# Performance work log

Hardware: AMD Instinct MI355X
Metric: run time of the kernel (lower is better)

Reference implementation:

```python
import jax, jax.numpy as jnp
import numpy as np

N = 100000
E = 1600000
C_IN = 32
C_OUT = 64
B = 4
VOXEL_SIZE = 0.0625
GRID_LO, GRID_HI = 0.0, 1.0
VOX = int((GRID_HI - GRID_LO) / VOXEL_SIZE)  # 16
R_CORR = GRID_HI - GRID_LO  # r_correction = max(grid_scale) - min(grid_scale) = 1


def setup_inputs() -> dict:
    key = jax.random.key(0)
    k1, k2, k3, k4, k5, k6 = jax.random.split(key, 6)
    x = jax.random.normal(k1, (N, C_IN), dtype=jnp.float32)
    edge_index = jax.random.randint(k2, (2, E), 0, N, dtype=jnp.int32)
    pos = jax.random.uniform(k3, (N, 2), dtype=jnp.float32)
    batch = jnp.sort(jax.random.randint(k4, (N,), 0, B, dtype=jnp.int32))
    W = jax.random.normal(k5, (C_OUT, 4 * C_IN), dtype=jnp.float32) / np.sqrt(4 * C_IN)
    b = jax.random.normal(k6, (C_OUT,), dtype=jnp.float32) * 0.01
    return {"x": x, "edge_index": edge_index, "pos": pos, "batch": batch, "W": W, "b": b}


def dpo_conv(x, edge_index, pos, W, b):
    row, col = edge_index[0], edge_index[1]  # j = source, i = target (PyG default flow)
    pos_i, pos_j = pos[col], pos[row]        # [E, 2]
    v_i, v_j = x[col], x[row]                # [E, C_IN]
    diff = pos_i - pos_j                     # [E, 2]
    r2 = jnp.sum(diff * diff, axis=1, keepdims=True)  # [E, 1]
    w = diff * R_CORR / (r2 + 0.01)          # [E, 2] -> columns are diff_x, diff_y
    v_diff = v_i - v_j                       # [E, C_IN]
    # message f: [E, 3*C_IN]
    f = jnp.concatenate([v_diff * w[:, 0:1], v_diff * w[:, 1:2], v_j], axis=1)
    # scatter-mean into target nodes i = col
    summed = jax.ops.segment_sum(f, col, num_segments=N)            # [N, 3*C_IN]
    cnt = jax.ops.segment_sum(jnp.ones((E, 1), f.dtype), col, num_segments=N)
    prop = summed / jnp.maximum(cnt, 1.0)
    prop = jnp.concatenate([prop, x], axis=1)  # [N, 4*C_IN]
    return prop @ W.T + b


def reference(x, edge_index, pos, batch, W, b):
    h = jax.nn.relu(dpo_conv(x, edge_index, pos, W, b))  # [N, C_OUT]
    # voxel_grid: per-graph voxel cluster ids, then max_pool per cluster (dense grid)
    vox = jnp.clip(jnp.floor((pos - GRID_LO) / VOXEL_SIZE).astype(jnp.int32), 0, VOX - 1)
    cluster = batch * (VOX * VOX) + vox[:, 1] * VOX + vox[:, 0]     # [N]
    n_clusters = B * VOX * VOX
    pooled_x = jax.ops.segment_max(h, cluster, num_segments=n_clusters)  # [B*V^2, C_OUT]
    pooled_x = jnp.where(jnp.isfinite(pooled_x), pooled_x, 0.0)          # empty voxels -> 0
    pos_sum = jax.ops.segment_sum(pos, cluster, num_segments=n_clusters)
    node_cnt = jax.ops.segment_sum(jnp.ones((N, 1), pos.dtype), cluster, num_segments=n_clusters)
    pooled_pos = pos_sum / jnp.maximum(node_cnt, 1.0)                    # mean pos per voxel
    return pooled_x, pooled_pos, pos, batch
```

## Files before the change

kernel.cpp:

```cpp
#include <hip/hip_runtime.h>

#define NN 100000
#define NE 1600000
#define CAP 64
#define NCLUST 1024
#define OUT_POOLED_POS 65536
#define OUT_POS        67584
#define OUT_BATCH      267584

__global__ __launch_bounds__(256) void fill_kernel(const int* __restrict__ ei,
                                                   int* __restrict__ wp,
                                                   int* __restrict__ csr)
{
    int t = blockIdx.x * 256 + threadIdx.x;
    int e0 = t * 4;
    if (e0 + 3 < NE) {
        int4 r = *(const int4*)(ei + e0);
        int4 c = *(const int4*)(ei + NE + e0);
        int s;
        s = atomicAdd(&wp[c.x], 1); if (s < CAP) csr[(size_t)c.x * CAP + s] = r.x;
        s = atomicAdd(&wp[c.y], 1); if (s < CAP) csr[(size_t)c.y * CAP + s] = r.y;
        s = atomicAdd(&wp[c.z], 1); if (s < CAP) csr[(size_t)c.z * CAP + s] = r.z;
        s = atomicAdd(&wp[c.w], 1); if (s < CAP) csr[(size_t)c.w * CAP + s] = r.w;
    } else {
        for (int e = e0; e < NE; ++e) {
            int c = ei[NE + e];
            int s = atomicAdd(&wp[c], 1);
            if (s < CAP) csr[(size_t)c * CAP + s] = ei[e];
        }
    }
}

__global__ __launch_bounds__(1024, 8) void fused_kernel(
    const float4* __restrict__ x4,
    const float2* __restrict__ pos2,
    const int* __restrict__ batch,
    const float4* __restrict__ W4,
    const float* __restrict__ bv,
    const int* __restrict__ wp,
    const int* __restrict__ csr,
    float* __restrict__ out,
    float* __restrict__ pos_sum,
    float* __restrict__ node_cnt)
{
    __shared__ float4 Wt4[32 * 64];
    __shared__ float  bs[64];
    __shared__ float4 prop4[16][4][32];

    {
        int oc0 = threadIdx.x & 63;
        int k0  = threadIdx.x >> 6;
        Wt4[k0 * 64 + oc0]        = W4[oc0 * 32 + k0];
        Wt4[(k0 + 16) * 64 + oc0] = W4[oc0 * 32 + k0 + 16];
        if (threadIdx.x < 64) bs[threadIdx.x] = bv[threadIdx.x];
    }
    __syncthreads();

    const int wid  = threadIdx.x >> 6;
    const int lane = threadIdx.x & 63;
    const int q  = lane >> 4;
    const int g  = (lane >> 3) & 1;
    const int s  = lane & 7;
    const int oc = lane;
    const int nwaves = gridDim.x * 16;

    for (int wg = blockIdx.x * 16 + wid; wg * 4 < NN; wg += nwaves) {
        int n = wg * 4 + q;
        bool act = (n < NN);
        int nn = act ? n : 0;

        int cnt = wp[nn];
        int deg = act ? min(cnt, CAP) : 0;
        float4 vi = x4[(size_t)nn * 8 + s];
        float2 pi = pos2[nn];
        const int* bk = csr + (size_t)nn * CAP;

        int md = deg;
        md = max(md, __shfl_xor(md, 16));
        md = max(md, __shfl_xor(md, 32));

        float a0x=0,a0y=0,a0z=0,a0w=0;
        float a1x=0,a1y=0,a1z=0,a1w=0;
        float a2x=0,a2y=0,a2z=0,a2w=0;

        int k = g;
        bool p = (k < deg);
        int j = p ? bk[k] : nn;
        float m = p ? 1.0f : 0.0f;
        float2 pj = pos2[j];
        float4 vj = x4[(size_t)j * 8 + s];

        int iters = (md + 1) >> 1;
        for (int it = 0; it < iters; ++it) {
            int k2 = k + 2;
            bool p2 = (k2 < deg);
            int j2 = p2 ? bk[k2] : nn;
            float2 pjn = pos2[j2];
            float4 vjn = x4[(size_t)j2 * 8 + s];

            float dx = pi.x - pj.x, dy = pi.y - pj.y;
            float inv = m * __builtin_amdgcn_rcpf(dx * dx + dy * dy + 0.01f);
            float wx = dx * inv, wy = dy * inv;
            float vdx = vi.x - vj.x, vdy = vi.y - vj.y;
            float vdz = vi.z - vj.z, vdw = vi.w - vj.w;
            a0x += vdx * wx; a0y += vdy * wx; a0z += vdz * wx; a0w += vdw * wx;
            a1x += vdx * wy; a1y += vdy * wy; a1z += vdz * wy; a1w += vdw * wy;
            a2x += vj.x * m; a2y += vj.y * m; a2z += vj.z * m; a2w += vj.w * m;

            k = k2; m = p2 ? 1.0f : 0.0f;
            pj = pjn; vj = vjn;
        }

        a0x += __shfl_xor(a0x, 8); a0y += __shfl_xor(a0y, 8);
        a0z += __shfl_xor(a0z, 8); a0w += __shfl_xor(a0w, 8);
        a1x += __shfl_xor(a1x, 8); a1y += __shfl_xor(a1y, 8);
        a1z += __shfl_xor(a1z, 8); a1w += __shfl_xor(a1w, 8);
        a2x += __shfl_xor(a2x, 8); a2y += __shfl_xor(a2y, 8);
        a2z += __shfl_xor(a2z, 8); a2w += __shfl_xor(a2w, 8);

        float invd = 1.0f / fmaxf((float)cnt, 1.0f);
        if (g == 0) {
            prop4[wid][q][s]      = make_float4(a0x*invd, a0y*invd, a0z*invd, a0w*invd);
            prop4[wid][q][8 + s]  = make_float4(a1x*invd, a1y*invd, a1z*invd, a1w*invd);
            prop4[wid][q][16 + s] = make_float4(a2x*invd, a2y*invd, a2z*invd, a2w*invd);
            prop4[wid][q][24 + s] = vi;
        }
        asm volatile("s_waitcnt lgkmcnt(0)" ::: "memory");

        float bb = bs[oc];
        float acc0 = bb, acc1 = bb, acc2 = bb, acc3 = bb;
        #pragma unroll 8
        for (int k4 = 0; k4 < 32; ++k4) {
            float4 w  = Wt4[k4 * 64 + oc];
            float4 p0 = prop4[wid][0][k4];
            float4 p1 = prop4[wid][1][k4];
            float4 p2 = prop4[wid][2][k4];
            float4 p3 = prop4[wid][3][k4];
            acc0 += w.x*p0.x + w.y*p0.y + w.z*p0.z + w.w*p0.w;
            acc1 += w.x*p1.x + w.y*p1.y + w.z*p1.z + w.w*p1.w;
            acc2 += w.x*p2.x + w.y*p2.y + w.z*p2.z + w.w*p2.w;
            acc3 += w.x*p3.x + w.y*p3.y + w.z*p3.z + w.w*p3.w;
        }

        float accq[4] = {acc0, acc1, acc2, acc3};
        #pragma unroll
        for (int qq = 0; qq < 4; ++qq) {
            int n2 = wg * 4 + qq;
            if (n2 < NN) {
                float h = fmaxf(accq[qq], 0.0f);
                float2 pp = pos2[n2];
                int b = batch[n2];
                int vx = min(max((int)floorf(pp.x * 16.0f), 0), 15);
                int vy = min(max((int)floorf(pp.y * 16.0f), 0), 15);
                int cl = b * 256 + vy * 16 + vx;
                atomicMax((unsigned int*)(out + (size_t)cl * 64 + oc),
                          __float_as_uint(h));
                if (oc == qq) {
                    *(float2*)(out + OUT_POS + 2 * (size_t)n2) = pp;
                    out[OUT_BATCH + n2] = (float)b;
                    atomicAdd(pos_sum + 2 * cl,     pp.x);
                    atomicAdd(pos_sum + 2 * cl + 1, pp.y);
                    atomicAdd(node_cnt + cl, 1.0f);
                }
            }
        }
        asm volatile("s_waitcnt lgkmcnt(0)" ::: "memory");
    }
}

__global__ void finalize_kernel(const float* __restrict__ pos_sum,
                                const float* __restrict__ node_cnt,
                                float* __restrict__ out_pooled_pos)
{
    int c = blockIdx.x * blockDim.x + threadIdx.x;
    if (c >= NCLUST) return;
    float inv = 1.0f / fmaxf(node_cnt[c], 1.0f);
    out_pooled_pos[2 * c]     = pos_sum[2 * c] * inv;
    out_pooled_pos[2 * c + 1] = pos_sum[2 * c + 1] * inv;
}

extern "C" void kernel_launch(void* const* d_in, const int* in_sizes, int n_in,
                              void* d_out, int out_size, void* d_ws, size_t ws_size,
                              hipStream_t stream)
{
    const float* x     = (const float*)d_in[0];
    const int*   ei    = (const int*)d_in[1];
    const float* pos   = (const float*)d_in[2];
    const int*   batch = (const int*)d_in[3];
    const float* W     = (const float*)d_in[4];
    const float* bvec  = (const float*)d_in[5];
    float* out = (float*)d_out;

    int* wp  = (int*)d_ws;
    int* csr = wp + NN;
    float* pos_sum  = (float*)(csr + (size_t)NN * CAP);
    float* node_cnt = pos_sum + 2 * NCLUST;

    hipMemsetAsync(wp, 0, NN * sizeof(int), stream);
    hipMemsetAsync(pos_sum, 0, 3 * NCLUST * sizeof(float), stream);
    hipMemsetAsync(d_out, 0, (size_t)NCLUST * 64 * sizeof(float), stream);

    fill_kernel<<<(NE / 4 + 255) / 256, 256, 0, stream>>>(ei, wp, csr);

    fused_kernel<<<512, 1024, 0, stream>>>(
        (const float4*)x, (const float2*)pos, batch,
        (const float4*)W, bvec, wp, csr, out, pos_sum, node_cnt);

    finalize_kernel<<<(NCLUST + 255) / 256, 256, 0, stream>>>(
        pos_sum, node_cnt, out + NCLUST * 64);
}
```

Baseline: 293.0 us.

## Launch one wave per node group, deepen index prefetch, skip redundant atomicMax

The grid-stride loop in the fused kernel is replaced by a one-shot mapping: 1563 blocks of 16 waves, each wave handling one group of 4 nodes. The neighbour loop now prefetches the neighbour index two steps ahead and the features one step ahead, so the dependent csr→x load chain is shortened. Before the pooling atomicMax, the current value is read and the atomic is skipped when it cannot raise the max, cutting atomic traffic. Separately, the CSR fill uses nontemporal stores. The cost is that each block reloads W into shared memory more often, and plain reads race with concurrent atomics, which is benign only because max is monotonic.

```diff
diff --git a/kernel.cpp b/kernel.cpp
--- a/kernel.cpp
+++ b/kernel.cpp
@@ -18,15 +18,19 @@
         int4 r = *(const int4*)(ei + e0);
         int4 c = *(const int4*)(ei + NE + e0);
         int s;
-        s = atomicAdd(&wp[c.x], 1); if (s < CAP) csr[(size_t)c.x * CAP + s] = r.x;
-        s = atomicAdd(&wp[c.y], 1); if (s < CAP) csr[(size_t)c.y * CAP + s] = r.y;
-        s = atomicAdd(&wp[c.z], 1); if (s < CAP) csr[(size_t)c.z * CAP + s] = r.z;
-        s = atomicAdd(&wp[c.w], 1); if (s < CAP) csr[(size_t)c.w * CAP + s] = r.w;
+        s = atomicAdd(&wp[c.x], 1);
+        if (s < CAP) __builtin_nontemporal_store(r.x, csr + (size_t)c.x * CAP + s);
+        s = atomicAdd(&wp[c.y], 1);
+        if (s < CAP) __builtin_nontemporal_store(r.y, csr + (size_t)c.y * CAP + s);
+        s = atomicAdd(&wp[c.z], 1);
+        if (s < CAP) __builtin_nontemporal_store(r.z, csr + (size_t)c.z * CAP + s);
+        s = atomicAdd(&wp[c.w], 1);
+        if (s < CAP) __builtin_nontemporal_store(r.w, csr + (size_t)c.w * CAP + s);
     } else {
         for (int e = e0; e < NE; ++e) {
             int c = ei[NE + e];
             int s = atomicAdd(&wp[c], 1);
-            if (s < CAP) csr[(size_t)c * CAP + s] = ei[e];
+            if (s < CAP) __builtin_nontemporal_store(ei[e], csr + (size_t)c * CAP + s);
         }
     }
 }
@@ -62,109 +66,116 @@
     const int g  = (lane >> 3) & 1;
     const int s  = lane & 7;
     const int oc = lane;
-    const int nwaves = gridDim.x * 16;
-
-    for (int wg = blockIdx.x * 16 + wid; wg * 4 < NN; wg += nwaves) {
-        int n = wg * 4 + q;
-        bool act = (n < NN);
-        int nn = act ? n : 0;
-
-        int cnt = wp[nn];
-        int deg = act ? min(cnt, CAP) : 0;
-        float4 vi = x4[(size_t)nn * 8 + s];
-        float2 pi = pos2[nn];
-        const int* bk = csr + (size_t)nn * CAP;
-
-        int md = deg;
-        md = max(md, __shfl_xor(md, 16));
-        md = max(md, __shfl_xor(md, 32));
-
-        float a0x=0,a0y=0,a0z=0,a0w=0;
-        float a1x=0,a1y=0,a1z=0,a1w=0;
-        float a2x=0,a2y=0,a2z=0,a2w=0;
-
-        int k = g;
-        bool p = (k < deg);
-        int j = p ? bk[k] : nn;
-        float m = p ? 1.0f : 0.0f;
-        float2 pj = pos2[j];
-        float4 vj = x4[(size_t)j * 8 + s];
-
-        int iters = (md + 1) >> 1;
-        for (int it = 0; it < iters; ++it) {
-            int k2 = k + 2;
-            bool p2 = (k2 < deg);
-            int j2 = p2 ? bk[k2] : nn;
-            float2 pjn = pos2[j2];
-            float4 vjn = x4[(size_t)j2 * 8 + s];
-
-            float dx = pi.x - pj.x, dy = pi.y - pj.y;
-            float inv = m * __builtin_amdgcn_rcpf(dx * dx + dy * dy + 0.01f);
-            float wx = dx * inv, wy = dy * inv;
-            float vdx = vi.x - vj.x, vdy = vi.y - vj.y;
-            float vdz = vi.z - vj.z, vdw = vi.w - vj.w;
-            a0x += vdx * wx; a0y += vdy * wx; a0z += vdz * wx; a0w += vdw * wx;
-            a1x += vdx * wy; a1y += vdy * wy; a1z += vdz * wy; a1w += vdw * wy;
-            a2x += vj.x * m; a2y += vj.y * m; a2z += vj.z * m; a2w += vj.w * m;
-
-            k = k2; m = p2 ? 1.0f : 0.0f;
-            pj = pjn; vj = vjn;
-        }
-
-        a0x += __shfl_xor(a0x, 8); a0y += __shfl_xor(a0y, 8);
-        a0z += __shfl_xor(a0z, 8); a0w += __shfl_xor(a0w, 8);
-        a1x += __shfl_xor(a1x, 8); a1y += __shfl_xor(a1y, 8);
-        a1z += __shfl_xor(a1z, 8); a1w += __shfl_xor(a1w, 8);
-        a2x += __shfl_xor(a2x, 8); a2y += __shfl_xor(a2y, 8);
-        a2z += __shfl_xor(a2z, 8); a2w += __shfl_xor(a2w, 8);
-
-        float invd = 1.0f / fmaxf((float)cnt, 1.0f);
-        if (g == 0) {
-            prop4[wid][q][s]      = make_float4(a0x*invd, a0y*invd, a0z*invd, a0w*invd);
-            prop4[wid][q][8 + s]  = make_float4(a1x*invd, a1y*invd, a1z*invd, a1w*invd);
-            prop4[wid][q][16 + s] = make_float4(a2x*invd, a2y*invd, a2z*invd, a2w*invd);
-            prop4[wid][q][24 + s] = vi;
-        }
-        asm volatile("s_waitcnt lgkmcnt(0)" ::: "memory");
-
-        float bb = bs[oc];
-        float acc0 = bb, acc1 = bb, acc2 = bb, acc3 = bb;
-        #pragma unroll 8
-        for (int k4 = 0; k4 < 32; ++k4) {
-            float4 w  = Wt4[k4 * 64 + oc];
-            float4 p0 = prop4[wid][0][k4];
-            float4 p1 = prop4[wid][1][k4];
-            float4 p2 = prop4[wid][2][k4];
-            float4 p3 = prop4[wid][3][k4];
-            acc0 += w.x*p0.x + w.y*p0.y + w.z*p0.z + w.w*p0.w;
-            acc1 += w.x*p1.x + w.y*p1.y + w.z*p1.z + w.w*p1.w;
-            acc2 += w.x*p2.x + w.y*p2.y + w.z*p2.z + w.w*p2.w;
-            acc3 += w.x*p3.x + w.y*p3.y + w.z*p3.z + w.w*p3.w;
-        }
-
-        float accq[4] = {acc0, acc1, acc2, acc3};
-        #pragma unroll
-        for (int qq = 0; qq < 4; ++qq) {
-            int n2 = wg * 4 + qq;
-            if (n2 < NN) {
-                float h = fmaxf(accq[qq], 0.0f);
-                float2 pp = pos2[n2];
-                int b = batch[n2];
-                int vx = min(max((int)floorf(pp.x * 16.0f), 0), 15);
-                int vy = min(max((int)floorf(pp.y * 16.0f), 0), 15);
-                int cl = b * 256 + vy * 16 + vx;
-                atomicMax((unsigned int*)(out + (size_t)cl * 64 + oc),
-                          __float_as_uint(h));
-                if (oc == qq) {
-                    *(float2*)(out + OUT_POS + 2 * (size_t)n2) = pp;
-                    out[OUT_BATCH + n2] = (float)b;
-                    atomicAdd(pos_sum + 2 * cl,     pp.x);
-                    atomicAdd(pos_sum + 2 * cl + 1, pp.y);
-                    atomicAdd(node_cnt + cl, 1.0f);
-                }
+
+    int wg = blockIdx.x * 16 + wid;
+    if (wg * 4 >= NN) return;
+
+    int n = wg * 4 + q;
+    bool act = (n < NN);
+    int nn = act ? n : 0;
+
+    int cnt = wp[nn];
+    int deg = act ? min(cnt, CAP) : 0;
+    float4 vi = x4[(size_t)nn * 8 + s];
+    float2 pi = pos2[nn];
+    const int* bk = csr + (size_t)nn * CAP;
+
+    int md = deg;
+    md = max(md, __shfl_xor(md, 16));
+    md = max(md, __shfl_xor(md, 32));
+
+    float a0x=0,a0y=0,a0z=0,a0w=0;
+    float a1x=0,a1y=0,a1z=0,a1w=0;
+    float a2x=0,a2y=0,a2z=0,a2w=0;
+
+    int k0i = g;
+    bool p0 = (k0i < deg);
+    int j0 = p0 ? bk[k0i] : nn;
+    float m0 = p0 ? 1.0f : 0.0f;
+    float2 pj0 = pos2[j0];
+    float4 vj0 = x4[(size_t)j0 * 8 + s];
+
+    int k1 = g + 2;
+    bool p1 = (k1 < deg);
+    int j1 = p1 ? bk[k1] : nn;
+    float m1 = p1 ? 1.0f : 0.0f;
+
+    int iters = (md + 1) >> 1;
+    for (int it = 0; it < iters; ++it) {
+        int k2 = k1 + 2;
+        bool p2 = (k2 < deg);
+        int j2 = p2 ? bk[k2] : nn;
+        float m2 = p2 ? 1.0f : 0.0f;
+        float2 pjn = pos2[j1];
+        float4 vjn = x4[(size_t)j1 * 8 + s];
+
+        float dx = pi.x - pj0.x, dy = pi.y - pj0.y;
+        float inv = m0 * __builtin_amdgcn_rcpf(dx * dx + dy * dy + 0.01f);
+        float wx = dx * inv, wy = dy * inv;
+        float vdx = vi.x - vj0.x, vdy = vi.y - vj0.y;
+        float vdz = vi.z - vj0.z, vdw = vi.w - vj0.w;
+        a0x += vdx * wx; a0y += vdy * wx; a0z += vdz * wx; a0w += vdw * wx;
+        a1x += vdx * wy; a1y += vdy * wy; a1z += vdz * wy; a1w += vdw * wy;
+        a2x += vj0.x * m0; a2y += vj0.y * m0; a2z += vj0.z * m0; a2w += vj0.w * m0;
+
+        pj0 = pjn; vj0 = vjn; m0 = m1;
+        j1 = j2; m1 = m2; k1 = k2;
+    }
+
+    a0x += __shfl_xor(a0x, 8); a0y += __shfl_xor(a0y, 8);
+    a0z += __shfl_xor(a0z, 8); a0w += __shfl_xor(a0w, 8);
+    a1x += __shfl_xor(a1x, 8); a1y += __shfl_xor(a1y, 8);
+    a1z += __shfl_xor(a1z, 8); a1w += __shfl_xor(a1w, 8);
+    a2x += __shfl_xor(a2x, 8); a2y += __shfl_xor(a2y, 8);
+    a2z += __shfl_xor(a2z, 8); a2w += __shfl_xor(a2w, 8);
+
+    float invd = 1.0f / fmaxf((float)cnt, 1.0f);
+    if (g == 0) {
+        prop4[wid][q][s]      = make_float4(a0x*invd, a0y*invd, a0z*invd, a0w*invd);
+        prop4[wid][q][8 + s]  = make_float4(a1x*invd, a1y*invd, a1z*invd, a1w*invd);
+        prop4[wid][q][16 + s] = make_float4(a2x*invd, a2y*invd, a2z*invd, a2w*invd);
+        prop4[wid][q][24 + s] = vi;
+    }
+    asm volatile("s_waitcnt lgkmcnt(0)" ::: "memory");
+
+    float bb = bs[oc];
+    float acc0 = bb, acc1 = bb, acc2 = bb, acc3 = bb;
+    #pragma unroll 8
+    for (int k4 = 0; k4 < 32; ++k4) {
+        float4 w  = Wt4[k4 * 64 + oc];
+        float4 pp0 = prop4[wid][0][k4];
+        float4 pp1 = prop4[wid][1][k4];
+        float4 pp2 = prop4[wid][2][k4];
+        float4 pp3 = prop4[wid][3][k4];
+        acc0 += w.x*pp0.x + w.y*pp0.y + w.z*pp0.z + w.w*pp0.w;
+        acc1 += w.x*pp1.x + w.y*pp1.y + w.z*pp1.z + w.w*pp1.w;
+        acc2 += w.x*pp2.x + w.y*pp2.y + w.z*pp2.z + w.w*pp2.w;
+        acc3 += w.x*pp3.x + w.y*pp3.y + w.z*pp3.z + w.w*pp3.w;
+    }
+
+    float accq[4] = {acc0, acc1, acc2, acc3};
+    #pragma unroll
+    for (int qq = 0; qq < 4; ++qq) {
+        int n2 = wg * 4 + qq;
+        if (n2 < NN) {
+            float h = fmaxf(accq[qq], 0.0f);
+            float2 pp = pos2[n2];
+            int b = batch[n2];
+            int vx = min(max((int)floorf(pp.x * 16.0f), 0), 15);
+            int vy = min(max((int)floorf(pp.y * 16.0f), 0), 15);
+            int cl = b * 256 + vy * 16 + vx;
+            unsigned int* tgt = (unsigned int*)(out + (size_t)cl * 64 + oc);
+            unsigned int prev = *tgt;
+            unsigned int cur  = __float_as_uint(h);
+            if (cur > prev) atomicMax(tgt, cur);
+            if (oc == qq) {
+                *(float2*)(out + OUT_POS + 2 * (size_t)n2) = pp;
+                out[OUT_BATCH + n2] = (float)b;
+                atomicAdd(pos_sum + 2 * cl,     pp.x);
+                atomicAdd(pos_sum + 2 * cl + 1, pp.y);
+                atomicAdd(node_cnt + cl, 1.0f);
             }
         }
-        asm volatile("s_waitcnt lgkmcnt(0)" ::: "memory");
     }
 }
 
@@ -202,7 +213,7 @@
 
     fill_kernel<<<(NE / 4 + 255) / 256, 256, 0, stream>>>(ei, wp, csr);
 
-    fused_kernel<<<512, 1024, 0, stream>>>(
+    fused_kernel<<<1563, 1024, 0, stream>>>(
         (const float4*)x, (const float2*)pos, batch,
         (const float4*)W, bvec, wp, csr, out, pos_sum, node_cnt);
 
```

New measurement: 319.8 us. 9.1% more time.
